# Optimization experiments

Hardware: AMD Instinct MI355X
Metric: run time of the kernel (lower is better)

Reference implementation:

```python
import jax, jax.numpy as jnp
import numpy as np

EPS = 1e-6


def setup_inputs() -> dict:
    key = jax.random.key(0)
    kx, ky = jax.random.split(key)
    B, C, H, W = 8, 128, 48, 64
    x = jax.random.normal(kx, (B, C, H, W), dtype=jnp.float32)
    y = jax.random.normal(ky, (B, C, H, W), dtype=jnp.float32)
    return {"x": x, "y": y}


def reference(x, y):
    # x, y: (b, c, h, w)
    b, c, h, w = x.shape
    # torch: x.transpose(2,3).view(b,c,h*w) -> x flattened w-major,
    #        so output channel k = v*h + u corresponds to x[:, :, u, v].
    # corr5[b, v, u, i, j] = sum_c x[b,c,u,v] * y[b,c,i,j]
    corr = jnp.einsum('bcuv,bcij->bvuij', x, y)
    corr = corr.reshape(b, w * h, h, w)  # channel k = v*h + u
    # normalization: ReLU then L2-normalize over the h*w channel dim
    corr = jax.nn.relu(corr)
    norm = jnp.sqrt(jnp.sum(corr * corr, axis=1, keepdims=True) + EPS)
    return corr / norm
```

## Files before the change

kernel.cpp:

```cpp
#include <hip/hip_runtime.h>
#include <hip/hip_bf16.h>

#define NB 8
#define NC 128
#define NH 48
#define NW 64
#define NS 3072
#define EPSF 1e-6f

#define GLOBAL_AS __attribute__((address_space(1)))
#define LDS_AS __attribute__((address_space(3)))

typedef __bf16 bf16x8 __attribute__((ext_vector_type(8)));
typedef float f32x4 __attribute__((ext_vector_type(4)));

__global__ __launch_bounds__(256) void transpose_both(
    const float* __restrict__ x, const float* __restrict__ y,
    __hip_bfloat16* __restrict__ AT, __hip_bfloat16* __restrict__ BT) {
  __shared__ float tile[32][65];
  const int id = blockIdx.x;
  const int b = id & 7;
  const int which = (id >> 3) & 1;
  const int rr = id >> 4;
  const int f0 = (rr % 96) * 32, c0 = (rr / 96) * 64;
  const float* src = which ? y : x;
  __hip_bfloat16* dst = which ? BT : AT;
  const int t = threadIdx.x;

  const int fi = t & 31, ci0 = t >> 5;
  const float* sp = src + ((size_t)b * NC + c0) * NS + f0;
#pragma unroll
  for (int i = 0; i < 8; ++i) {
    int ci = ci0 + i * 8;
    tile[fi][ci] = sp[(size_t)ci * NS + fi];
  }
  __syncthreads();

  const int co = t & 63, fo0 = t >> 6;
#pragma unroll
  for (int i = 0; i < 8; ++i) {
    int fo = fo0 + i * 4;
    int f = f0 + fo;
    int k = which ? f : ((f & 63) * NH + (f >> 6));
    dst[((size_t)b * NS + k) * NC + c0 + co] = __float2bfloat16(tile[fo][co]);
  }
}

template <int CPW>
__device__ __forceinline__ void stage_tile(const char* gsrc, char* ldst,
                                           int wid, int lane) {
  const int lr = lane >> 4, lg = lane & 15;
#pragma unroll
  for (int i = 0; i < CPW; ++i) {
    int c = wid * CPW + i;
    int row = c * 4 + lr;
    int g = lg ^ (row & 7);
    __builtin_amdgcn_global_load_lds(
        (const GLOBAL_AS unsigned*)(gsrc + row * 256 + g * 16),
        (LDS_AS unsigned*)(ldst + c * 1024), 16, 0, 0);
  }
}

__device__ __forceinline__ void gemm_acc(const char* As, const char* Bs,
                                         float cs[2], int wm, int wn, int l15,
                                         int kg) {
  f32x4 acc[4][2] = {};
  const int rx = l15 & 7;
#pragma unroll
  for (int kk = 0; kk < 4; ++kk) {
    int g = (kk * 4 + kg) ^ rx;
    bf16x8 a[4], bb[2];
#pragma unroll
    for (int mi = 0; mi < 4; ++mi)
      a[mi] = *(const bf16x8*)(As + (wm * 64 + mi * 16 + l15) * 256 + g * 16);
#pragma unroll
    for (int ni = 0; ni < 2; ++ni)
      bb[ni] = *(const bf16x8*)(Bs + (wn * 32 + ni * 16 + l15) * 256 + g * 16);
#pragma unroll
    for (int mi = 0; mi < 4; ++mi)
#pragma unroll
      for (int ni = 0; ni < 2; ++ni)
        acc[mi][ni] = __builtin_amdgcn_mfma_f32_16x16x32_bf16(
            a[mi], bb[ni], acc[mi][ni], 0, 0, 0);
  }
#pragma unroll
  for (int ni = 0; ni < 2; ++ni)
#pragma unroll
    for (int mi = 0; mi < 4; ++mi)
#pragma unroll
      for (int r = 0; r < 4; ++r) {
        float v = fmaxf(acc[mi][ni][r], 0.f);
        cs[ni] += v * v;
      }
}

__global__ __launch_bounds__(512, 1) void corr_part_p(
    const __hip_bfloat16* __restrict__ AT,
    const __hip_bfloat16* __restrict__ BT, float* __restrict__ part) {
  __shared__ char smem[98304];
  char* Bs = smem + 65536;
  const int id = blockIdx.x;
  const int b = id & 7;
  const int tl = id >> 3;
  const int nt = tl >> 2, mq = tl & 3;
  const int t = threadIdx.x;
  const int lane = t & 63, wid = t >> 6;
  const int wm = wid >> 2, wn = wid & 3;
  const int l15 = lane & 15, kg = lane >> 4;

  const char* Ab = (const char*)(AT + ((size_t)b * NS + mq * 768) * NC);
  const char* Bg = (const char*)(BT + ((size_t)b * NS + nt * 128) * NC);

  stage_tile<4>(Bg, Bs, wid, lane);
  stage_tile<4>(Ab, smem, wid, lane);
  asm volatile("s_waitcnt vmcnt(0)" ::: "memory");
  __builtin_amdgcn_sched_barrier(0);
  __builtin_amdgcn_s_barrier();

  float cs[2] = {0.f, 0.f};
  int cur = 0;
#pragma unroll 1
  for (int i = 0; i < 6; ++i) {
    if (i + 1 < 6)
      stage_tile<4>(Ab + (size_t)(i + 1) * 32768, smem + ((cur ^ 1) * 32768),
                    wid, lane);
    gemm_acc(smem + cur * 32768, Bs, cs, wm, wn, l15, kg);
    asm volatile("s_waitcnt vmcnt(0)" ::: "memory");
    __builtin_amdgcn_sched_barrier(0);
    __builtin_amdgcn_s_barrier();
    cur ^= 1;
  }

#pragma unroll
  for (int ni = 0; ni < 2; ++ni) {
    cs[ni] += __shfl_xor(cs[ni], 16, 64);
    cs[ni] += __shfl_xor(cs[ni], 32, 64);
  }
  float* csum = (float*)smem;
  if (kg == 0) {
#pragma unroll
    for (int ni = 0; ni < 2; ++ni)
      csum[wm * 128 + wn * 32 + ni * 16 + l15] = cs[ni];
  }
  __syncthreads();
  if (t < 128) {
    float s = csum[t] + csum[128 + t];
    part[(size_t)mq * (NB * NS) + (size_t)b * NS + nt * 128 + t] = s;
  }
}

__global__ __launch_bounds__(256, 2) void corr_out(
    const __hip_bfloat16* __restrict__ AT,
    const __hip_bfloat16* __restrict__ BT, const float* __restrict__ part_in,
    float* __restrict__ out) {
  __shared__ char smem[66560];
  float* rnc = (float*)(smem + 65536);
  const int id = blockIdx.x;
  const int b = id & 7;
  const int tl = id >> 3;
  const int mt = tl / 24, nt = tl - mt * 24;
  const int t = threadIdx.x;
  const int lane = t & 63, wid = t >> 6;
  const int wm = wid >> 1, wn = wid & 1;
  const int l15 = lane & 15, kg = lane >> 4;

  const char* Ag = (const char*)(AT + ((size_t)b * NS + mt * 128) * NC);
  const char* Bg = (const char*)(BT + ((size_t)b * NS + nt * 128) * NC);
  stage_tile<8>(Ag, smem, wid, lane);
  stage_tile<8>(Bg, smem + 32768, wid, lane);
  if (t < 128) {
    float s = 0.f;
#pragma unroll
    for (int q = 0; q < 4; ++q)
      s += part_in[(size_t)q * (NB * NS) + (size_t)b * NS + nt * 128 + t];
    rnc[t] = rsqrtf(s + EPSF);
  }
  __syncthreads();

  f32x4 acc[4][4] = {};
  const int rx = l15 & 7;
#pragma unroll
  for (int kk = 0; kk < 4; ++kk) {
    int g = (kk * 4 + kg) ^ rx;
    bf16x8 a[4], bb[4];
#pragma unroll
    for (int mi = 0; mi < 4; ++mi)
      a[mi] = *(const bf16x8*)(smem + (wm * 64 + mi * 16 + l15) * 256 + g * 16);
#pragma unroll
    for (int ni = 0; ni < 4; ++ni)
      bb[ni] = *(const bf16x8*)(smem + 32768 +
                                (wn * 64 + ni * 16 + l15) * 256 + g * 16);
#pragma unroll
    for (int mi = 0; mi < 4; ++mi)
#pragma unroll
      for (int ni = 0; ni < 4; ++ni)
        acc[mi][ni] = __builtin_amdgcn_mfma_f32_16x16x32_bf16(
            a[mi], bb[ni], acc[mi][ni], 0, 0, 0);
  }

  float rnv[4];
#pragma unroll
  for (int ni = 0; ni < 4; ++ni) rnv[ni] = rnc[wn * 64 + ni * 16 + l15];
  __syncthreads();

  float* tf = (float*)smem;
#pragma unroll
  for (int mi = 0; mi < 4; ++mi)
#pragma unroll
    for (int ni = 0; ni < 4; ++ni)
#pragma unroll
      for (int r = 0; r < 4; ++r) {
        int row = wm * 64 + mi * 16 + kg * 4 + r;
        int col = wn * 64 + ni * 16 + l15;
        tf[row * 129 + col] = fmaxf(acc[mi][ni][r], 0.f) * rnv[ni];
      }
  __syncthreads();

  float* ob = out + (size_t)b * NS * NS + (size_t)(mt * 128) * NS + nt * 128;
  const int rsub = t >> 5, c4 = (t & 31) * 4;
#pragma unroll
  for (int it = 0; it < 16; ++it) {
    int row = it * 8 + rsub;
    f32x4 v = *(const f32x4*)&tf[row * 129 + c4];
    __builtin_nontemporal_store(v, (f32x4*)&ob[(size_t)row * NS + c4]);
  }
}

extern "C" void kernel_launch(void* const* d_in, const int* in_sizes, int n_in,
                              void* d_out, int out_size, void* d_ws,
                              size_t ws_size, hipStream_t stream) {
  const float* x = (const float*)d_in[0];
  const float* y = (const float*)d_in[1];
  float* out = (float*)d_out;
  char* ws = (char*)d_ws;

  const size_t AT_OFF = 0;
  const size_t BT_OFF = 6291456;
  const size_t PART_OFF = 12582912;
  const size_t NEED = 12976128;
  if (ws_size < NEED) return;

  __hip_bfloat16* AT = (__hip_bfloat16*)(ws + AT_OFF);
  __hip_bfloat16* BT = (__hip_bfloat16*)(ws + BT_OFF);
  float* part = (float*)(ws + PART_OFF);

  transpose_both<<<dim3(3072), dim3(256), 0, stream>>>(x, y, AT, BT);
  corr_part_p<<<dim3(768), dim3(512), 0, stream>>>(AT, BT, part);
  corr_out<<<dim3(4608), dim3(256), 0, stream>>>(AT, BT, part, out);
}
```

Baseline: 99.19 us.

## Make output kernel persistent, pipelining tile staging with normalized stores

Replaces the 4608-block output GEMM+normalize kernel with a 256-block, 512-thread persistent kernel. Each block loops over 18 output tiles of 128x128, keeping its A tile resident across six B tiles. It prefetches the next B (and sometimes A) tile into LDS while writing the current tile to global memory. The inverse norms for all its columns are computed once per block. This is meant to cut launch/tail overhead and redundant staging and to overlap loads with the large output store stream. The cost is only one block per CU, which may leave fewer stores in flight.

```diff
diff --git a/kernel.cpp b/kernel.cpp
--- a/kernel.cpp
+++ b/kernel.cpp
@@ -149,80 +149,112 @@
   }
 }
 
-__global__ __launch_bounds__(256, 2) void corr_out(
+__global__ __launch_bounds__(512, 1) void corr_out_p(
     const __hip_bfloat16* __restrict__ AT,
     const __hip_bfloat16* __restrict__ BT, const float* __restrict__ part_in,
     float* __restrict__ out) {
-  __shared__ char smem[66560];
-  float* rnc = (float*)(smem + 65536);
+  __shared__ char smem[136192];
+  float* tf = (float*)(smem + 65536);
+  float* rnc = (float*)(smem + 65536 + 67584);
   const int id = blockIdx.x;
   const int b = id & 7;
-  const int tl = id >> 3;
-  const int mt = tl / 24, nt = tl - mt * 24;
+  const int q = id >> 3;
+  const int mg = q >> 2, ng = q & 3;
   const int t = threadIdx.x;
   const int lane = t & 63, wid = t >> 6;
-  const int wm = wid >> 1, wn = wid & 1;
+  const int wm = wid >> 2, wn = wid & 3;
   const int l15 = lane & 15, kg = lane >> 4;
 
-  const char* Ag = (const char*)(AT + ((size_t)b * NS + mt * 128) * NC);
-  const char* Bg = (const char*)(BT + ((size_t)b * NS + nt * 128) * NC);
-  stage_tile<8>(Ag, smem, wid, lane);
-  stage_tile<8>(Bg, smem + 32768, wid, lane);
-  if (t < 128) {
+  for (int v = t; v < 768; v += 512) {
     float s = 0.f;
 #pragma unroll
-    for (int q = 0; q < 4; ++q)
-      s += part_in[(size_t)q * (NB * NS) + (size_t)b * NS + nt * 128 + t];
-    rnc[t] = rsqrtf(s + EPSF);
-  }
-  __syncthreads();
-
-  f32x4 acc[4][4] = {};
-  const int rx = l15 & 7;
-#pragma unroll
-  for (int kk = 0; kk < 4; ++kk) {
-    int g = (kk * 4 + kg) ^ rx;
-    bf16x8 a[4], bb[4];
-#pragma unroll
-    for (int mi = 0; mi < 4; ++mi)
-      a[mi] = *(const bf16x8*)(smem + (wm * 64 + mi * 16 + l15) * 256 + g * 16);
-#pragma unroll
-    for (int ni = 0; ni < 4; ++ni)
-      bb[ni] = *(const bf16x8*)(smem + 32768 +
-                                (wn * 64 + ni * 16 + l15) * 256 + g * 16);
-#pragma unroll
-    for (int mi = 0; mi < 4; ++mi)
-#pragma unroll
-      for (int ni = 0; ni < 4; ++ni)
-        acc[mi][ni] = __builtin_amdgcn_mfma_f32_16x16x32_bf16(
-            a[mi], bb[ni], acc[mi][ni], 0, 0, 0);
-  }
-
-  float rnv[4];
-#pragma unroll
-  for (int ni = 0; ni < 4; ++ni) rnv[ni] = rnc[wn * 64 + ni * 16 + l15];
-  __syncthreads();
-
-  float* tf = (float*)smem;
-#pragma unroll
-  for (int mi = 0; mi < 4; ++mi)
-#pragma unroll
-    for (int ni = 0; ni < 4; ++ni)
-#pragma unroll
-      for (int r = 0; r < 4; ++r) {
-        int row = wm * 64 + mi * 16 + kg * 4 + r;
-        int col = wn * 64 + ni * 16 + l15;
-        tf[row * 129 + col] = fmaxf(acc[mi][ni][r], 0.f) * rnv[ni];
+    for (int qq = 0; qq < 4; ++qq)
+      s += part_in[(size_t)qq * (NB * NS) + (size_t)b * NS + ng * 768 + v];
+    rnc[v] = rsqrtf(s + EPSF);
+  }
+  const char* Abase = (const char*)(AT + (size_t)b * NS * NC);
+  const char* Bbase = (const char*)(BT + (size_t)b * NS * NC);
+  stage_tile<4>(Abase + (size_t)(mg * 3) * 32768, smem, wid, lane);
+  stage_tile<4>(Bbase + (size_t)(ng * 6) * 32768, smem + 32768, wid, lane);
+  asm volatile("s_waitcnt vmcnt(0) lgkmcnt(0)" ::: "memory");
+  __builtin_amdgcn_sched_barrier(0);
+  __builtin_amdgcn_s_barrier();
+
+#pragma unroll 1
+  for (int k = 0; k < 18; ++k) {
+    const int j = k % 6;
+    f32x4 acc[4][2] = {};
+    {
+      const int rx = l15 & 7;
+#pragma unroll
+      for (int kk = 0; kk < 4; ++kk) {
+        int g = (kk * 4 + kg) ^ rx;
+        bf16x8 a[4], bb[2];
+#pragma unroll
+        for (int mi = 0; mi < 4; ++mi)
+          a[mi] =
+              *(const bf16x8*)(smem + (wm * 64 + mi * 16 + l15) * 256 + g * 16);
+#pragma unroll
+        for (int ni = 0; ni < 2; ++ni)
+          bb[ni] = *(const bf16x8*)(smem + 32768 +
+                                    (wn * 32 + ni * 16 + l15) * 256 + g * 16);
+#pragma unroll
+        for (int mi = 0; mi < 4; ++mi)
+#pragma unroll
+          for (int ni = 0; ni < 2; ++ni)
+            acc[mi][ni] = __builtin_amdgcn_mfma_f32_16x16x32_bf16(
+                a[mi], bb[ni], acc[mi][ni], 0, 0, 0);
       }
-  __syncthreads();
-
-  float* ob = out + (size_t)b * NS * NS + (size_t)(mt * 128) * NS + nt * 128;
-  const int rsub = t >> 5, c4 = (t & 31) * 4;
-#pragma unroll
-  for (int it = 0; it < 16; ++it) {
-    int row = it * 8 + rsub;
-    f32x4 v = *(const f32x4*)&tf[row * 129 + c4];
-    __builtin_nontemporal_store(v, (f32x4*)&ob[(size_t)row * NS + c4]);
+    }
+    __builtin_amdgcn_s_barrier();
+
+    if (k + 1 < 18) {
+      const int k1 = k + 1;
+      if (k1 % 6 == 0)
+        stage_tile<4>(Abase + (size_t)(mg * 3 + k1 / 6) * 32768, smem, wid,
+                      lane);
+      stage_tile<4>(Bbase + (size_t)(ng * 6 + k1 % 6) * 32768, smem + 32768,
+                    wid, lane);
+    }
+
+    {
+      float rnv[2];
+#pragma unroll
+      for (int ni = 0; ni < 2; ++ni)
+        rnv[ni] = rnc[j * 128 + wn * 32 + ni * 16 + l15];
+#pragma unroll
+      for (int mi = 0; mi < 4; ++mi)
+#pragma unroll
+        for (int ni = 0; ni < 2; ++ni)
+#pragma unroll
+          for (int r = 0; r < 4; ++r) {
+            int row = wm * 64 + mi * 16 + kg * 4 + r;
+            int col = wn * 32 + ni * 16 + l15;
+            tf[row * 132 + col] = fmaxf(acc[mi][ni][r], 0.f) * rnv[ni];
+          }
+    }
+    asm volatile("s_waitcnt lgkmcnt(0)" ::: "memory");
+    __builtin_amdgcn_sched_barrier(0);
+    __builtin_amdgcn_s_barrier();
+
+    {
+      const int mt = mg * 3 + k / 6, nt = ng * 6 + j;
+      float* ob =
+          out + (size_t)b * NS * NS + (size_t)(mt * 128) * NS + nt * 128;
+      const int r0 = t >> 5, c4 = (t & 31) * 4;
+#pragma unroll
+      for (int it = 0; it < 8; ++it) {
+        int row = it * 16 + r0;
+        f32x4 v = *(const f32x4*)&tf[row * 132 + c4];
+        __builtin_nontemporal_store(v, (f32x4*)&ob[(size_t)row * NS + c4]);
+      }
+    }
+
+    if (k + 1 < 18) {
+      asm volatile("s_waitcnt vmcnt(8)" ::: "memory");
+      __builtin_amdgcn_sched_barrier(0);
+      __builtin_amdgcn_s_barrier();
+    }
   }
 }
 
@@ -246,5 +278,5 @@
 
   transpose_both<<<dim3(3072), dim3(256), 0, stream>>>(x, y, AT, BT);
   corr_part_p<<<dim3(768), dim3(512), 0, stream>>>(AT, BT, part);
-  corr_out<<<dim3(4608), dim3(256), 0, stream>>>(AT, BT, part, out);
-}
+  corr_out_p<<<dim3(256), dim3(512), 0, stream>>>(AT, BT, part, out);
+}
```

Measured after the change: 105.0 us. 5.8% more time.
